# Optimization experiments

Measured on AMD Instinct MI355X. Metric: run time of the kernel, lower is better.

The kernel has to match this reference:

```python
import jax, jax.numpy as jnp
import numpy as np

H = W = 2048        # voxel grid
P0 = 0.1            # occupancy density
EPS = 1e-5          # BatchNorm eps (torch default)


def _grid(rs, cs):
    g = np.full((H, W), -1, np.int64)
    g[rs, cs] = np.arange(rs.size)
    return g


def _conv_map(g, rs, cs, s):
    # kernel map for 3x3 conv at tensor stride s: offsets {-s,0,s}^2, -1 = missing neighbor
    maps = []
    for dr in (-s, 0, s):
        for dc in (-s, 0, s):
            r2, c2 = rs + dr, cs + dc
            ok = (r2 >= 0) & (r2 < H) & (c2 >= 0) & (c2 < W)
            m = np.full(rs.size, -1, np.int64)
            m[ok] = g[r2[ok], c2[ok]]
            maps.append(m)
    return np.stack(maps, 1)  # [N, 9]


def _pool_map(g, rs, cs, s):
    # 2x2 max pool stride 2 at tensor stride s: out coords = floor to multiples of 2s
    out = np.unique(np.stack([rs - rs % (2 * s), cs - cs % (2 * s)], 1), axis=0)
    maps = []
    for dr in (0, s):
        for dc in (0, s):
            r2, c2 = out[:, 0] + dr, out[:, 1] + dc
            ok = (r2 < H) & (c2 < W)
            m = np.full(out.shape[0], -1, np.int64)
            m[ok] = g[r2[ok], c2[ok]]
            maps.append(m)
    return out, np.stack(maps, 1)  # coords, [N_out, 4]


def _build_maps():
    rng = np.random.default_rng(0)
    n0 = int(H * W * P0)
    flat = rng.choice(H * W, size=n0, replace=False)
    flat.sort()
    rs0, cs0 = np.divmod(flat, W)
    g0 = _grid(rs0, cs0)
    nbr0 = _conv_map(g0, rs0, cs0, 1)
    c1, pmap1 = _pool_map(g0, rs0, cs0, 1)
    g1 = _grid(c1[:, 0], c1[:, 1])
    nbr1 = _conv_map(g1, c1[:, 0], c1[:, 1], 2)
    c2, pmap2 = _pool_map(g1, c1[:, 0], c1[:, 1], 2)
    return n0, nbr0, pmap1, nbr1, pmap2, c2.shape[0]


def setup_inputs() -> dict:
    n0, nbr0, pmap1, nbr1, pmap2, n2 = _build_maps()
    key = jax.random.key(0)
    k0, k1, k2, k3 = jax.random.split(key, 4)
    f0 = jax.random.normal(k0, (n0, 1), jnp.float32)
    W1 = jax.random.normal(k1, (9, 1, 8), jnp.float32) * 0.3
    W2 = jax.random.normal(k2, (9, 8, 16), jnp.float32) * 0.12
    Wfc = jax.random.normal(k3, (16, 2), jnp.float32) * 0.25
    return dict(
        f0=f0, W1=W1, b1=jnp.zeros((8,), jnp.float32),
        gamma1=jnp.ones((8,), jnp.float32), beta1=jnp.zeros((8,), jnp.float32),
        W2=W2, b2=jnp.zeros((16,), jnp.float32),
        gamma2=jnp.ones((16,), jnp.float32), beta2=jnp.zeros((16,), jnp.float32),
        Wfc=Wfc, bfc=jnp.zeros((2,), jnp.float32),
        nbr0=jnp.asarray(nbr0), pmap1=jnp.asarray(pmap1),
        nbr1=jnp.asarray(nbr1), pmap2=jnp.asarray(pmap2),
    )


def _sparse_conv(f, nbr, Wk, b):
    # gather-matmul-scatter: missing neighbors contribute zero
    n = f.shape[0]
    fpad = jnp.concatenate([f, jnp.zeros((1, f.shape[1]), f.dtype)], 0)
    g = fpad[jnp.where(nbr < 0, n, nbr)]  # [N_out, 9, C_in]
    return jnp.einsum('nkc,kcd->nd', g, Wk) + b


def _bn_relu(x, gamma, beta):
    mu = x.mean(0)
    var = x.var(0)  # biased, as torch BN normalization
    return jax.nn.relu((x - mu) * jax.lax.rsqrt(var + EPS) * gamma + beta)


def _max_pool(f, pmap):
    # max over existing children only (every output has >= 1 child)
    n = f.shape[0]
    fpad = jnp.concatenate([f, jnp.full((1, f.shape[1]), -jnp.inf, f.dtype)], 0)
    return fpad[jnp.where(pmap < 0, n, pmap)].max(1)


def reference(f0, W1, b1, gamma1, beta1, W2, b2, gamma2, beta2, Wfc, bfc,
              nbr0, pmap1, nbr1, pmap2):
    x = _bn_relu(_sparse_conv(f0, nbr0, W1, b1), gamma1, beta1)
    x = _max_pool(x, pmap1)
    x = _bn_relu(_sparse_conv(x, nbr1, W2, b2), gamma2, beta2)
    x = _max_pool(x, pmap2)
    return x @ Wfc + bfc
```

## Files before the change

kernel.cpp:

```cpp
#include <hip/hip_runtime.h>

#define EPS 1e-5f
#define NSLOT 64

__device__ __forceinline__ float waveReduceSum(float v) {
    #pragma unroll
    for (int off = 32; off > 0; off >>= 1)
        v += __shfl_down(v, off, 64);
    return v;
}

template <int NV>
__device__ __forceinline__ float statReduce(float (&v)[NV], int lane) {
    #pragma unroll
    for (int b = 0; (1 << b) < NV; ++b) {
        const int d = 1 << b;
        const bool hi = (lane >> b) & 1;
        #pragma unroll
        for (int i = 0; i < (NV >> (b + 1)); ++i) {
            float kept = hi ? v[2 * i + 1] : v[2 * i];
            float sent = hi ? v[2 * i] : v[2 * i + 1];
            float recv = __shfl_xor(sent, d, 64);
            v[i] = kept + recv;
        }
    }
    float r = v[0];
    #pragma unroll
    for (int d = NV; d < 64; d <<= 1)
        r += __shfl_xor(r, d, 64);
    return r;
}

__global__ __launch_bounds__(256) void k_zero(float4* __restrict__ slots) {
    const float4 z4 = {0.f, 0.f, 0.f, 0.f};
    #pragma unroll
    for (int q = 0; q < 4; ++q)
        slots[q * 256 + threadIdx.x] = z4;
}

__global__ __launch_bounds__(256) void k_conv1(
        const float* __restrict__ f0, const float* __restrict__ W1,
        const float* __restrict__ b1, const int* __restrict__ nbr0,
        float* __restrict__ x1, float* __restrict__ slots, int n0) {
    __shared__ float sred[16];
    int t = threadIdx.x;
    int lane = t & 63;
    if (t < 16) sred[t] = 0.f;
    __syncthreads();

    int n = blockIdx.x * blockDim.x + t;
    bool valid = (n < n0);
    int nn = valid ? n : (n0 - 1);

    int idx[9];
    #pragma unroll
    for (int k = 0; k < 9; ++k) idx[k] = nbr0[(size_t)nn * 9 + k];
    float v[9];
    #pragma unroll
    for (int k = 0; k < 9; ++k) {
        float f = f0[idx[k] >= 0 ? idx[k] : 0];
        v[k] = (idx[k] >= 0) ? f : 0.f;
    }

    float acc[8];
    #pragma unroll
    for (int c = 0; c < 8; ++c) acc[c] = b1[c];
    #pragma unroll
    for (int k = 0; k < 9; ++k)
        #pragma unroll
        for (int c = 0; c < 8; ++c) acc[c] = fmaf(v[k], W1[k * 8 + c], acc[c]);

    if (valid) {
        float4 lo = {acc[0], acc[1], acc[2], acc[3]};
        float4 hi = {acc[4], acc[5], acc[6], acc[7]};
        float4* dst = (float4*)(x1 + (size_t)n * 8);
        dst[0] = lo; dst[1] = hi;
    } else {
        #pragma unroll
        for (int c = 0; c < 8; ++c) acc[c] = 0.f;
    }

    float red[16];
    #pragma unroll
    for (int c = 0; c < 8; ++c) {
        red[c] = acc[c];
        red[8 + c] = acc[c] * acc[c];
    }
    float tot = statReduce<16>(red, lane);
    if (lane < 16) atomicAdd(&sred[lane], tot);
    __syncthreads();
    if (t < 16) {
        float* slot = slots + (size_t)(blockIdx.x & (NSLOT - 1)) * 64;
        atomicAdd(&slot[t], sred[t]);
    }
}

__global__ __launch_bounds__(256) void k_pool1(
        const float* __restrict__ x1, const int* __restrict__ pmap1,
        const float* __restrict__ slots, const float* __restrict__ gamma1,
        const float* __restrict__ beta1, float* __restrict__ p1,
        int n1, float invn) {
    __shared__ float sstat[16];
    int t = threadIdx.x;
    if (t < 64) {
        const float4* s4 = (const float4*)(slots + (size_t)t * 64);
        float4 a = s4[0], b = s4[1], c4 = s4[2], d = s4[3];
        float vals[16] = {a.x, a.y, a.z, a.w, b.x, b.y, b.z, b.w,
                          c4.x, c4.y, c4.z, c4.w, d.x, d.y, d.z, d.w};
        #pragma unroll
        for (int c = 0; c < 16; ++c) {
            float s = waveReduceSum(vals[c]);
            if (t == 0) sstat[c] = s;
        }
    }
    __syncthreads();

    int i = blockIdx.x * blockDim.x + t;
    if (i >= n1) return;

    float m[8], sc[8], bb[8];
    #pragma unroll
    for (int c = 0; c < 8; ++c) {
        float mu  = sstat[c] * invn;
        float var = sstat[8 + c] * invn - mu * mu;
        m[c]  = mu;
        sc[c] = rsqrtf(var + EPS) * gamma1[c];
        bb[c] = beta1[c];
    }

    int4 pm = ((const int4*)pmap1)[i];
    int idx[4] = {pm.x, pm.y, pm.z, pm.w};
    float best[8];
    #pragma unroll
    for (int c = 0; c < 8; ++c) best[c] = 0.f;
    #pragma unroll
    for (int k = 0; k < 4; ++k) {
        int j = idx[k] >= 0 ? idx[k] : 0;
        const float4* src = (const float4*)(x1 + (size_t)j * 8);
        float4 lo = src[0], hi = src[1];
        float v[8] = {lo.x, lo.y, lo.z, lo.w, hi.x, hi.y, hi.z, hi.w};
        #pragma unroll
        for (int c = 0; c < 8; ++c) {
            float z = fmaxf(fmaf(v[c] - m[c], sc[c], bb[c]), 0.f);
            z = (idx[k] >= 0) ? z : 0.f;
            best[c] = fmaxf(best[c], z);
        }
    }
    float4 lo = {best[0], best[1], best[2], best[3]};
    float4 hi = {best[4], best[5], best[6], best[7]};
    float4* dst = (float4*)(p1 + (size_t)i * 8);
    dst[0] = lo; dst[1] = hi;
}

__global__ __launch_bounds__(256, 6) void k_conv2(
        const float* __restrict__ p1, const float* __restrict__ W2,
        const float* __restrict__ b2, const int* __restrict__ nbr1,
        float* __restrict__ x2, float* __restrict__ slots, int n1) {
    __shared__ float sred[32];
    int t = threadIdx.x;
    int lane = t & 63;
    if (t < 32) sred[t] = 0.f;
    __syncthreads();

    int n = blockIdx.x * blockDim.x + t;
    bool valid = (n < n1);
    int nn = valid ? n : (n1 - 1);

    int idx[9];
    #pragma unroll
    for (int k = 0; k < 9; ++k) idx[k] = nbr1[(size_t)nn * 9 + k];

    float acc[16];
    #pragma unroll
    for (int c = 0; c < 16; ++c) acc[c] = b2[c];

    #pragma unroll
    for (int k = 0; k < 9; ++k) {
        const float4* src = (const float4*)(p1 + (size_t)(idx[k] >= 0 ? idx[k] : 0) * 8);
        float4 lo = src[0], hi = src[1];
        if (idx[k] < 0) {
            lo = make_float4(0.f, 0.f, 0.f, 0.f);
            hi = make_float4(0.f, 0.f, 0.f, 0.f);
        }
        float g[8] = {lo.x, lo.y, lo.z, lo.w, hi.x, hi.y, hi.z, hi.w};
        #pragma unroll
        for (int ci = 0; ci < 8; ++ci) {
            #pragma unroll
            for (int c = 0; c < 16; ++c)
                acc[c] = fmaf(g[ci], W2[(k * 8 + ci) * 16 + c], acc[c]);
        }
    }

    if (valid) {
        float4* dst = (float4*)(x2 + (size_t)n * 16);
        #pragma unroll
        for (int q4 = 0; q4 < 4; ++q4) {
            float4 v = {acc[q4 * 4], acc[q4 * 4 + 1], acc[q4 * 4 + 2], acc[q4 * 4 + 3]};
            dst[q4] = v;
        }
    } else {
        #pragma unroll
        for (int c = 0; c < 16; ++c) acc[c] = 0.f;
    }

    float red[32];
    #pragma unroll
    for (int c = 0; c < 16; ++c) {
        red[c] = acc[c];
        red[16 + c] = acc[c] * acc[c];
    }
    float tot = statReduce<32>(red, lane);
    if (lane < 32) atomicAdd(&sred[lane], tot);
    __syncthreads();
    if (t < 32) {
        float* slot = slots + (size_t)(blockIdx.x & (NSLOT - 1)) * 64;
        atomicAdd(&slot[16 + t], sred[t]);
    }
}

__global__ __launch_bounds__(256) void k_pool2_fc(
        const float* __restrict__ x2, const int* __restrict__ pmap2,
        const float* __restrict__ slots, const float* __restrict__ gamma2,
        const float* __restrict__ beta2, const float* __restrict__ Wfc,
        const float* __restrict__ bfc, float* __restrict__ out,
        int n2, float invn) {
    __shared__ float sstat[32];
    int t = threadIdx.x;
    if (t < 64) {
        const float4* s4 = (const float4*)(slots + (size_t)t * 64 + 16);
        float vals[32];
        #pragma unroll
        for (int q = 0; q < 8; ++q) {
            float4 a = s4[q];
            vals[q * 4 + 0] = a.x; vals[q * 4 + 1] = a.y;
            vals[q * 4 + 2] = a.z; vals[q * 4 + 3] = a.w;
        }
        #pragma unroll
        for (int c = 0; c < 32; ++c) {
            float s = waveReduceSum(vals[c]);
            if (t == 0) sstat[c] = s;
        }
    }
    __syncthreads();

    int i = blockIdx.x * blockDim.x + t;
    if (i >= n2) return;

    float m[16], sc[16], bb[16];
    #pragma unroll
    for (int c = 0; c < 16; ++c) {
        float mu  = sstat[c] * invn;
        float var = sstat[16 + c] * invn - mu * mu;
        m[c]  = mu;
        sc[c] = rsqrtf(var + EPS) * gamma2[c];
        bb[c] = beta2[c];
    }

    int4 pm = ((const int4*)pmap2)[i];
    int idx[4] = {pm.x, pm.y, pm.z, pm.w};
    float best[16];
    #pragma unroll
    for (int c = 0; c < 16; ++c) best[c] = 0.f;
    #pragma unroll
    for (int k = 0; k < 4; ++k) {
        int j = idx[k] >= 0 ? idx[k] : 0;
        const float4* src = (const float4*)(x2 + (size_t)j * 16);
        #pragma unroll
        for (int q4 = 0; q4 < 4; ++q4) {
            float4 v4 = src[q4];
            float v[4] = {v4.x, v4.y, v4.z, v4.w};
            #pragma unroll
            for (int c = 0; c < 4; ++c) {
                int cc = q4 * 4 + c;
                float z = fmaxf(fmaf(v[c] - m[cc], sc[cc], bb[cc]), 0.f);
                z = (idx[k] >= 0) ? z : 0.f;
                best[cc] = fmaxf(best[cc], z);
            }
        }
    }
    float o0 = bfc[0], o1 = bfc[1];
    #pragma unroll
    for (int c = 0; c < 16; ++c) {
        o0 = fmaf(best[c], Wfc[c * 2 + 0], o0);
        o1 = fmaf(best[c], Wfc[c * 2 + 1], o1);
    }
    out[(size_t)i * 2 + 0] = o0;
    out[(size_t)i * 2 + 1] = o1;
}

extern "C" void kernel_launch(void* const* d_in, const int* in_sizes, int n_in,
                              void* d_out, int out_size, void* d_ws, size_t ws_size,
                              hipStream_t stream) {
    const float* f0     = (const float*)d_in[0];
    const float* W1     = (const float*)d_in[1];
    const float* b1     = (const float*)d_in[2];
    const float* gamma1 = (const float*)d_in[3];
    const float* beta1  = (const float*)d_in[4];
    const float* W2     = (const float*)d_in[5];
    const float* b2     = (const float*)d_in[6];
    const float* gamma2 = (const float*)d_in[7];
    const float* beta2  = (const float*)d_in[8];
    const float* Wfc    = (const float*)d_in[9];
    const float* bfc    = (const float*)d_in[10];
    const int*   nbr0   = (const int*)d_in[11];
    const int*   pmap1  = (const int*)d_in[12];
    const int*   nbr1   = (const int*)d_in[13];
    const int*   pmap2  = (const int*)d_in[14];

    const int n0 = in_sizes[0];
    const int n1 = in_sizes[12] / 4;
    const int n2 = in_sizes[14] / 4;

    float* ws    = (float*)d_ws;
    float* slots = ws;
    float* x1    = ws + (size_t)NSLOT * 64;
    float* p1    = x1 + (size_t)n0 * 8;
    float* x2    = p1 + (size_t)n1 * 8;

    const int B = 256;
    k_zero<<<1, B, 0, stream>>>((float4*)slots);
    k_conv1<<<(n0 + B - 1) / B, B, 0, stream>>>(f0, W1, b1, nbr0, x1, slots, n0);
    k_pool1<<<(n1 + B - 1) / B, B, 0, stream>>>(x1, pmap1, slots, gamma1, beta1, p1,
                                                n1, 1.0f / (float)n0);
    k_conv2<<<(n1 + B - 1) / B, B, 0, stream>>>(p1, W2, b2, nbr1, x2, slots, n1);
    k_pool2_fc<<<(n2 + B - 1) / B, B, 0, stream>>>(x2, pmap2, slots, gamma2, beta2,
                                                   Wfc, bfc, (float*)d_out,
                                                   n2, 1.0f / (float)n1);
}
```

Baseline: 70.65 us.

## Fuse conv1 with pool1 via per-parent max/min, defer BN1 into conv2

Conv1 now runs per pooled output, computing its existing children's conv outputs and storing per-channel max and min instead of writing the full x1 tensor. BN1+ReLU is applied inside conv2 by choosing max or min according to the sign of the BN scale, which removes the separate pool1 kernel and the x1 write and reread. Each pooled parent stores 16 floats instead of 8, so conv2's neighbor gathers read twice as much data. Conv1 work is regrouped by parent, which changes the order of its gathers.

```diff
diff --git a/kernel.cpp b/kernel.cpp
--- a/kernel.cpp
+++ b/kernel.cpp
@@ -2,6 +2,7 @@
 
 #define EPS 1e-5f
 #define NSLOT 64
+#define FLT_BIG 3.402823466e+38f
 
 __device__ __forceinline__ float waveReduceSum(float v) {
     #pragma unroll
@@ -38,70 +39,102 @@
         slots[q * 256 + threadIdx.x] = z4;
 }
 
-__global__ __launch_bounds__(256) void k_conv1(
+__global__ __launch_bounds__(256, 4) void k_conv1pool(
         const float* __restrict__ f0, const float* __restrict__ W1,
         const float* __restrict__ b1, const int* __restrict__ nbr0,
-        float* __restrict__ x1, float* __restrict__ slots, int n0) {
+        const int* __restrict__ pmap1, float* __restrict__ pmm,
+        float* __restrict__ slots, int n1) {
     __shared__ float sred[16];
     int t = threadIdx.x;
     int lane = t & 63;
     if (t < 16) sred[t] = 0.f;
     __syncthreads();
 
-    int n = blockIdx.x * blockDim.x + t;
-    bool valid = (n < n0);
-    int nn = valid ? n : (n0 - 1);
-
-    int idx[9];
-    #pragma unroll
-    for (int k = 0; k < 9; ++k) idx[k] = nbr0[(size_t)nn * 9 + k];
-    float v[9];
-    #pragma unroll
-    for (int k = 0; k < 9; ++k) {
-        float f = f0[idx[k] >= 0 ? idx[k] : 0];
-        v[k] = (idx[k] >= 0) ? f : 0.f;
-    }
-
-    float acc[8];
-    #pragma unroll
-    for (int c = 0; c < 8; ++c) acc[c] = b1[c];
-    #pragma unroll
-    for (int k = 0; k < 9; ++k)
-        #pragma unroll
-        for (int c = 0; c < 8; ++c) acc[c] = fmaf(v[k], W1[k * 8 + c], acc[c]);
+    int i = blockIdx.x * blockDim.x + t;
+    bool valid = (i < n1);
+    int icl = valid ? i : (n1 - 1);
+    int4 pm = ((const int4*)pmap1)[icl];
+    if (!valid) { pm.x = -1; pm.y = -1; pm.z = -1; pm.w = -1; }
+    int ch[4] = {pm.x, pm.y, pm.z, pm.w};
+
+    float maxv[8], minv[8], red[16];
+    #pragma unroll
+    for (int c = 0; c < 8; ++c) { maxv[c] = -FLT_BIG; minv[c] = FLT_BIG; }
+    #pragma unroll
+    for (int c = 0; c < 16; ++c) red[c] = 0.f;
+
+    #pragma unroll
+    for (int p = 0; p < 2; ++p) {
+        int c0 = ch[2 * p], c1 = ch[2 * p + 1];
+        int j0 = c0 >= 0 ? c0 : 0;
+        int j1 = c1 >= 0 ? c1 : 0;
+        int idx0[9], idx1[9];
+        #pragma unroll
+        for (int k = 0; k < 9; ++k) idx0[k] = nbr0[(size_t)j0 * 9 + k];
+        #pragma unroll
+        for (int k = 0; k < 9; ++k) idx1[k] = nbr0[(size_t)j1 * 9 + k];
+        float v0[9], v1[9];
+        #pragma unroll
+        for (int k = 0; k < 9; ++k) {
+            int e = idx0[k]; float f = f0[e >= 0 ? e : 0]; v0[k] = e >= 0 ? f : 0.f;
+        }
+        #pragma unroll
+        for (int k = 0; k < 9; ++k) {
+            int e = idx1[k]; float f = f0[e >= 0 ? e : 0]; v1[k] = e >= 0 ? f : 0.f;
+        }
+        float a0[8], a1[8];
+        #pragma unroll
+        for (int c = 0; c < 8; ++c) { a0[c] = b1[c]; a1[c] = b1[c]; }
+        #pragma unroll
+        for (int k = 0; k < 9; ++k) {
+            #pragma unroll
+            for (int c = 0; c < 8; ++c) {
+                float w = W1[k * 8 + c];
+                a0[c] = fmaf(v0[k], w, a0[c]);
+                a1[c] = fmaf(v1[k], w, a1[c]);
+            }
+        }
+        if (c0 >= 0) {
+            #pragma unroll
+            for (int c = 0; c < 8; ++c) {
+                red[c] += a0[c]; red[8 + c] += a0[c] * a0[c];
+                maxv[c] = fmaxf(maxv[c], a0[c]); minv[c] = fminf(minv[c], a0[c]);
+            }
+        }
+        if (c1 >= 0) {
+            #pragma unroll
+            for (int c = 0; c < 8; ++c) {
+                red[c] += a1[c]; red[8 + c] += a1[c] * a1[c];
+                maxv[c] = fmaxf(maxv[c], a1[c]); minv[c] = fminf(minv[c], a1[c]);
+            }
+        }
+    }
 
     if (valid) {
-        float4 lo = {acc[0], acc[1], acc[2], acc[3]};
-        float4 hi = {acc[4], acc[5], acc[6], acc[7]};
-        float4* dst = (float4*)(x1 + (size_t)n * 8);
-        dst[0] = lo; dst[1] = hi;
-    } else {
-        #pragma unroll
-        for (int c = 0; c < 8; ++c) acc[c] = 0.f;
-    }
-
-    float red[16];
-    #pragma unroll
-    for (int c = 0; c < 8; ++c) {
-        red[c] = acc[c];
-        red[8 + c] = acc[c] * acc[c];
-    }
+        float4* dst = (float4*)(pmm + (size_t)i * 16);
+        dst[0] = make_float4(maxv[0], maxv[1], maxv[2], maxv[3]);
+        dst[1] = make_float4(maxv[4], maxv[5], maxv[6], maxv[7]);
+        dst[2] = make_float4(minv[0], minv[1], minv[2], minv[3]);
+        dst[3] = make_float4(minv[4], minv[5], minv[6], minv[7]);
+    }
+
     float tot = statReduce<16>(red, lane);
     if (lane < 16) atomicAdd(&sred[lane], tot);
     __syncthreads();
-    if (t < 16) {
-        float* slot = slots + (size_t)(blockIdx.x & (NSLOT - 1)) * 64;
-        atomicAdd(&slot[t], sred[t]);
-    }
-}
-
-__global__ __launch_bounds__(256) void k_pool1(
-        const float* __restrict__ x1, const int* __restrict__ pmap1,
-        const float* __restrict__ slots, const float* __restrict__ gamma1,
-        const float* __restrict__ beta1, float* __restrict__ p1,
-        int n1, float invn) {
+    if (t < 16)
+        atomicAdd(&slots[(size_t)(blockIdx.x & (NSLOT - 1)) * 64 + t], sred[t]);
+}
+
+__global__ __launch_bounds__(256, 6) void k_conv2(
+        const float* __restrict__ pmm, const float* __restrict__ W2,
+        const float* __restrict__ b2, const int* __restrict__ nbr1,
+        const float* __restrict__ gamma1, const float* __restrict__ beta1,
+        float* __restrict__ x2, float* __restrict__ slots, int n1, float invn0) {
+    __shared__ float sred[32];
     __shared__ float sstat[16];
     int t = threadIdx.x;
+    int lane = t & 63;
+    if (t < 32) sred[t] = 0.f;
     if (t < 64) {
         const float4* s4 = (const float4*)(slots + (size_t)t * 64);
         float4 a = s4[0], b = s4[1], c4 = s4[2], d = s4[3];
@@ -115,52 +148,15 @@
     }
     __syncthreads();
 
-    int i = blockIdx.x * blockDim.x + t;
-    if (i >= n1) return;
-
-    float m[8], sc[8], bb[8];
+    float bm[8], sc[8], bb[8];
     #pragma unroll
     for (int c = 0; c < 8; ++c) {
-        float mu  = sstat[c] * invn;
-        float var = sstat[8 + c] * invn - mu * mu;
-        m[c]  = mu;
+        float mu  = sstat[c] * invn0;
+        float var = sstat[8 + c] * invn0 - mu * mu;
+        bm[c] = mu;
         sc[c] = rsqrtf(var + EPS) * gamma1[c];
         bb[c] = beta1[c];
     }
-
-    int4 pm = ((const int4*)pmap1)[i];
-    int idx[4] = {pm.x, pm.y, pm.z, pm.w};
-    float best[8];
-    #pragma unroll
-    for (int c = 0; c < 8; ++c) best[c] = 0.f;
-    #pragma unroll
-    for (int k = 0; k < 4; ++k) {
-        int j = idx[k] >= 0 ? idx[k] : 0;
-        const float4* src = (const float4*)(x1 + (size_t)j * 8);
-        float4 lo = src[0], hi = src[1];
-        float v[8] = {lo.x, lo.y, lo.z, lo.w, hi.x, hi.y, hi.z, hi.w};
-        #pragma unroll
-        for (int c = 0; c < 8; ++c) {
-            float z = fmaxf(fmaf(v[c] - m[c], sc[c], bb[c]), 0.f);
-            z = (idx[k] >= 0) ? z : 0.f;
-            best[c] = fmaxf(best[c], z);
-        }
-    }
-    float4 lo = {best[0], best[1], best[2], best[3]};
-    float4 hi = {best[4], best[5], best[6], best[7]};
-    float4* dst = (float4*)(p1 + (size_t)i * 8);
-    dst[0] = lo; dst[1] = hi;
-}
-
-__global__ __launch_bounds__(256, 6) void k_conv2(
-        const float* __restrict__ p1, const float* __restrict__ W2,
-        const float* __restrict__ b2, const int* __restrict__ nbr1,
-        float* __restrict__ x2, float* __restrict__ slots, int n1) {
-    __shared__ float sred[32];
-    int t = threadIdx.x;
-    int lane = t & 63;
-    if (t < 32) sred[t] = 0.f;
-    __syncthreads();
 
     int n = blockIdx.x * blockDim.x + t;
     bool valid = (n < n1);
@@ -176,13 +172,18 @@
 
     #pragma unroll
     for (int k = 0; k < 9; ++k) {
-        const float4* src = (const float4*)(p1 + (size_t)(idx[k] >= 0 ? idx[k] : 0) * 8);
-        float4 lo = src[0], hi = src[1];
-        if (idx[k] < 0) {
-            lo = make_float4(0.f, 0.f, 0.f, 0.f);
-            hi = make_float4(0.f, 0.f, 0.f, 0.f);
-        }
-        float g[8] = {lo.x, lo.y, lo.z, lo.w, hi.x, hi.y, hi.z, hi.w};
+        const float4* base =
+            (const float4*)(pmm + (size_t)(idx[k] >= 0 ? idx[k] : 0) * 16);
+        float4 M0 = base[0], M1 = base[1], m0 = base[2], m1 = base[3];
+        float mx[8] = {M0.x, M0.y, M0.z, M0.w, M1.x, M1.y, M1.z, M1.w};
+        float mn[8] = {m0.x, m0.y, m0.z, m0.w, m1.x, m1.y, m1.z, m1.w};
+        float g[8];
+        #pragma unroll
+        for (int c = 0; c < 8; ++c) {
+            float pooled = (sc[c] >= 0.f) ? mx[c] : mn[c];
+            float z = fmaxf(fmaf(pooled - bm[c], sc[c], bb[c]), 0.f);
+            g[c] = (idx[k] >= 0) ? z : 0.f;
+        }
         #pragma unroll
         for (int ci = 0; ci < 8; ++ci) {
             #pragma unroll
@@ -195,7 +196,8 @@
         float4* dst = (float4*)(x2 + (size_t)n * 16);
         #pragma unroll
         for (int q4 = 0; q4 < 4; ++q4) {
-            float4 v = {acc[q4 * 4], acc[q4 * 4 + 1], acc[q4 * 4 + 2], acc[q4 * 4 + 3]};
+            float4 v = {acc[q4 * 4], acc[q4 * 4 + 1],
+                        acc[q4 * 4 + 2], acc[q4 * 4 + 3]};
             dst[q4] = v;
         }
     } else {
@@ -212,10 +214,8 @@
     float tot = statReduce<32>(red, lane);
     if (lane < 32) atomicAdd(&sred[lane], tot);
     __syncthreads();
-    if (t < 32) {
-        float* slot = slots + (size_t)(blockIdx.x & (NSLOT - 1)) * 64;
-        atomicAdd(&slot[16 + t], sred[t]);
-    }
+    if (t < 32)
+        atomicAdd(&slots[(size_t)(blockIdx.x & (NSLOT - 1)) * 64 + 16 + t], sred[t]);
 }
 
 __global__ __launch_bounds__(256) void k_pool2_fc(
@@ -313,16 +313,15 @@
 
     float* ws    = (float*)d_ws;
     float* slots = ws;
-    float* x1    = ws + (size_t)NSLOT * 64;
-    float* p1    = x1 + (size_t)n0 * 8;
-    float* x2    = p1 + (size_t)n1 * 8;
+    float* pmm   = ws + (size_t)NSLOT * 64;
+    float* x2    = pmm + (size_t)n1 * 16;
 
     const int B = 256;
     k_zero<<<1, B, 0, stream>>>((float4*)slots);
-    k_conv1<<<(n0 + B - 1) / B, B, 0, stream>>>(f0, W1, b1, nbr0, x1, slots, n0);
-    k_pool1<<<(n1 + B - 1) / B, B, 0, stream>>>(x1, pmap1, slots, gamma1, beta1, p1,
-                                                n1, 1.0f / (float)n0);
-    k_conv2<<<(n1 + B - 1) / B, B, 0, stream>>>(p1, W2, b2, nbr1, x2, slots, n1);
+    k_conv1pool<<<(n1 + B - 1) / B, B, 0, stream>>>(f0, W1, b1, nbr0, pmap1,
+                                                    pmm, slots, n1);
+    k_conv2<<<(n1 + B - 1) / B, B, 0, stream>>>(pmm, W2, b2, nbr1, gamma1, beta1,
+                                                x2, slots, n1, 1.0f / (float)n0);
     k_pool2_fc<<<(n2 + B - 1) / B, B, 0, stream>>>(x2, pmap2, slots, gamma2, beta2,
                                                    Wfc, bfc, (float*)d_out,
                                                    n2, 1.0f / (float)n1);
```

Measured after the change: 88.52 us. 1.25x slower.
